# Optimization experiments

Measured on AMD Instinct MI355X. Metric: run time of the kernel, lower is better.

Reference implementation:

```python
import jax, jax.numpy as jnp
import numpy as np

D_MODEL = 1024
N_HEADS = 16
HEAD_DIM = D_MODEL // N_HEADS
SCALE = float(np.sqrt(HEAD_DIM))
NEG_INF = -1e30


def setup_inputs() -> dict:
    key = jax.random.key(0)
    k1, k2, k3 = jax.random.split(key, 3)
    B, S = 4, 2048
    x = jax.random.normal(k1, (B, S, D_MODEL), dtype=jnp.float32)
    attention_mask = jnp.ones((B, S), dtype=jnp.int32)
    # torch Linear(d, 3d, bias=False): y = x @ W^T; store pre-transposed (d, 3d)
    w_qkv = jax.random.normal(k2, (D_MODEL, 3 * D_MODEL), dtype=jnp.float32) * (1.0 / np.sqrt(D_MODEL))
    w_out = jax.random.normal(k3, (D_MODEL, D_MODEL), dtype=jnp.float32) * (1.0 / np.sqrt(D_MODEL))
    return {"x": x, "attention_mask": attention_mask, "w_qkv": w_qkv, "w_out": w_out}


def reference(x, attention_mask, w_qkv, w_out):
    B, S, _ = x.shape
    qkv = jnp.einsum('bsd,de->bse', x, w_qkv)                     # (B,S,3D)
    qkv = qkv.reshape(B, S, 3, N_HEADS, HEAD_DIM)
    q = qkv[:, :, 0].transpose(0, 2, 1, 3)                        # (B,H,S,hd)
    k = qkv[:, :, 1].transpose(0, 2, 1, 3)
    v = qkv[:, :, 2].transpose(0, 2, 1, 3)

    scores = jnp.einsum('bhqd,bhkd->bhqk', q, k) / SCALE          # (B,H,S,S)
    causal_mask = jnp.triu(jnp.ones((S, S), dtype=bool), k=1)     # True above diag
    scores = jnp.where(causal_mask[None, None], NEG_INF, scores)
    pad_mask = (attention_mask == 0)[:, None, None, :]            # (B,1,1,S)
    scores = jnp.where(pad_mask, NEG_INF, scores)

    attn = jax.nn.softmax(scores, axis=-1)                        # dropout=0 (eval)
    out = jnp.einsum('bhqk,bhkd->bhqd', attn, v)                  # (B,H,S,hd)
    out = out.transpose(0, 2, 1, 3).reshape(B, S, D_MODEL)
    return jnp.einsum('bsd,de->bse', out, w_out)
```

## Files before the change

### kernel.cpp

```cpp
#include <hip/hip_runtime.h>


typedef __attribute__((ext_vector_type(8))) short bf16x8;
typedef __attribute__((ext_vector_type(8))) unsigned short u16x8;
typedef __attribute__((ext_vector_type(4))) unsigned short u16x4;
typedef __attribute__((ext_vector_type(4))) float f32x4;

#define MFMA16 __builtin_amdgcn_mfma_f32_16x16x32_bf16

#define GLDS(gp, lp) __builtin_amdgcn_global_load_lds( \
    (const __attribute__((address_space(1))) unsigned int*)(gp), \
    (__attribute__((address_space(3))) unsigned int*)(lp), 16, 0, 0)

__device__ __forceinline__ unsigned short f2bf(float f) {
    union { float f; unsigned int u; } v; v.f = f;
    unsigned int r = v.u + 0x7fffu + ((v.u >> 16) & 1u);
    return (unsigned short)(r >> 16);
}

__global__ void k_prep(const float* __restrict__ x, unsigned short* __restrict__ xb,
                       const int* __restrict__ mask, unsigned short* __restrict__ mb,
                       const float* __restrict__ wqkv, unsigned short* __restrict__ w1t,
                       const float* __restrict__ wout, unsigned short* __restrict__ w2t) {
    __shared__ float tile[32][33];
    const int bx = blockIdx.x;
    if (bx < 4096) {
        size_t i = ((size_t)bx * 256 + threadIdx.x) * 8;
        float4 f0 = *(const float4*)(x + i);
        float4 f1 = *(const float4*)(x + i + 4);
        u16x8 v;
        v[0] = f2bf(f0.x); v[1] = f2bf(f0.y); v[2] = f2bf(f0.z); v[3] = f2bf(f0.w);
        v[4] = f2bf(f1.x); v[5] = f2bf(f1.y); v[6] = f2bf(f1.z); v[7] = f2bf(f1.w);
        *(u16x8*)(xb + i) = v;
        if (bx < 32) {
            int j = bx * 256 + threadIdx.x;
            mb[j] = mask[j] ? (unsigned short)0x3F80 : (unsigned short)0;
        }
    } else {
        const int b2 = bx - 4096;
        const int cb = b2 & 127, rb = b2 >> 7;
        const float* in = (cb < 96) ? wqkv : wout;
        unsigned short* out = (cb < 96) ? w1t : w2t;
        const int C = (cb < 96) ? 3072 : 1024;
        const int c0 = ((cb < 96) ? cb : cb - 96) * 32;
        const int r0 = rb * 32;
        int tx = threadIdx.x & 31, ty = threadIdx.x >> 5;
        for (int i = ty; i < 32; i += 8)
            tile[i][tx] = in[(size_t)(r0 + i) * C + (c0 + tx)];
        __syncthreads();
        for (int i = ty; i < 32; i += 8)
            out[(size_t)(c0 + i) * 1024 + (r0 + tx)] = f2bf(tile[tx][i]);
    }
}

template <int MODE>
__global__ __launch_bounds__(256) void k_gemm_bt(
    const unsigned short* __restrict__ Ab,
    const unsigned short* __restrict__ Bt,
    float* __restrict__ Cf,
    unsigned short* __restrict__ qb,
    unsigned short* __restrict__ kb,
    unsigned short* __restrict__ vt,
    const int* __restrict__ mask,
    int N, int K)
{
    __shared__ __align__(16) unsigned short la[128 * 64];
    __shared__ __align__(16) unsigned short lb[128 * 64];
    const int t = threadIdx.x;
    const int m0 = blockIdx.y * 128, n0 = blockIdx.x * 128;
    const int w = t >> 6, lane = t & 63;
    const int wm = (w & 1) * 64, wn = (w >> 1) * 64;
    const int lr = lane & 15, lq = lane >> 4;
    const int lr7 = lr & 7;
    const int rowb = lane >> 3;
    const int g8 = (((lane & 7) - rowb) & 7) * 8;

    f32x4 acc[4][4];
    for (int i = 0; i < 4; ++i)
        for (int j = 0; j < 4; ++j)
            acc[i][j] = (f32x4){0.f, 0.f, 0.f, 0.f};

    for (int k0 = 0; k0 < K; k0 += 64) {
        #pragma unroll
        for (int r = 0; r < 4; ++r) {
            const int rg = w * 8 + r * 32;
            GLDS(&Ab[(size_t)(m0 + rg + rowb) * K + k0 + g8], &la[rg * 64]);
            GLDS(&Bt[(size_t)(n0 + rg + rowb) * K + k0 + g8], &lb[rg * 64]);
        }
        __syncthreads();
        #pragma unroll
        for (int ks = 0; ks < 2; ++ks) {
            const int pa = ((ks * 4 + lq + lr7) & 7) * 8;
            bf16x8 af[4], bg[4];
            #pragma unroll
            for (int i = 0; i < 4; ++i) {
                af[i] = *(const bf16x8*)&la[(wm + i * 16 + lr) * 64 + pa];
                bg[i] = *(const bf16x8*)&lb[(wn + i * 16 + lr) * 64 + pa];
            }
            #pragma unroll
            for (int i = 0; i < 4; ++i)
                #pragma unroll
                for (int j = 0; j < 4; ++j)
                    acc[i][j] = MFMA16(af[i], bg[j], acc[i][j], 0, 0, 0);
        }
        __syncthreads();
    }

    const float QSCALE = 0.18033688f;
    if (MODE == 0) {
        for (int i = 0; i < 4; ++i)
            for (int j = 0; j < 4; ++j)
                for (int r = 0; r < 4; ++r) {
                    int row = m0 + wm + i * 16 + lq * 4 + r;
                    int col = n0 + wn + j * 16 + lr;
                    Cf[(size_t)row * N + col] = acc[i][j][r];
                }
    } else {
        const int which = n0 >> 10;
        if (which < 2) {
            unsigned short* dst = which ? kb : qb;
            const float sc = which ? 1.0f : QSCALE;
            for (int i = 0; i < 4; ++i)
                for (int j = 0; j < 4; ++j)
                    for (int r = 0; r < 4; ++r) {
                        int row = m0 + wm + i * 16 + lq * 4 + r;
                        int col = n0 + wn + j * 16 + lr;
                        int h = (col >> 6) & 15, d = col & 63;
                        int b = row >> 11, s = row & 2047;
                        dst[((size_t)(b * 16 + h) * 2048 + s) * 64 + d] = f2bf(acc[i][j][r] * sc);
                    }
        } else {
            for (int i = 0; i < 4; ++i) {
                int s0 = m0 + wm + i * 16 + lq * 4;
                int b = s0 >> 11, s = s0 & 2047;
                int4 m4 = *(const int4*)&mask[b * 2048 + s];
                for (int j = 0; j < 4; ++j) {
                    int col = n0 + wn + j * 16 + lr;
                    int h = (col >> 6) & 15, d = col & 63;
                    u16x4 pv;
                    pv[0] = m4.x ? f2bf(acc[i][j][0]) : (unsigned short)0;
                    pv[1] = m4.y ? f2bf(acc[i][j][1]) : (unsigned short)0;
                    pv[2] = m4.z ? f2bf(acc[i][j][2]) : (unsigned short)0;
                    pv[3] = m4.w ? f2bf(acc[i][j][3]) : (unsigned short)0;
                    *(u16x4*)&vt[((size_t)(b * 16 + h) * 64 + d) * 2048 + s] = pv;
                }
            }
        }
    }
}

__global__ __launch_bounds__(512, 4) void k_attn(
    const unsigned short* __restrict__ qb,
    const unsigned short* __restrict__ kb,
    const unsigned short* __restrict__ vt,
    const unsigned short* __restrict__ maskbg,
    unsigned short* __restrict__ ao)
{
    __shared__ __align__(16) unsigned short kt_lds[2][64 * 64];
    __shared__ __align__(16) unsigned short vt_lds[2][64 * 64];
    __shared__ __align__(16) unsigned short plds[8][16 * 72];

    const int t = threadIdx.x;
    const int w = t >> 6, lane = t & 63;
    const int lr = lane & 15, lq = lane >> 4;
    const int lr7 = lr & 7;
    const int bh = blockIdx.y, b = bh >> 4, h = bh & 15;

    const unsigned short* qp = qb + (size_t)bh * 2048 * 64;
    const unsigned short* kp = kb + (size_t)bh * 2048 * 64;
    const unsigned short* vp = vt + (size_t)bh * 64 * 2048;
    const unsigned short* mbg = maskbg + b * 2048;
    unsigned short* pw = plds[w];

    const int rowb = lane >> 3, c8 = lane & 7;
    const int sc8 = (c8 ^ rowb) * 8;

    auto stage = [&](int c) {
        const int buf = c & 1;
        const int k0 = c * 64;
        const int rg = 8 * w;
        const int row = rg + rowb;
        GLDS(&kp[(size_t)(k0 + row) * 64 + sc8], &kt_lds[buf][rg * 64]);
        GLDS(&vp[(size_t)row * 2048 + k0 + sc8], &vt_lds[buf][rg * 64]);
    };

    for (int pass = 0; pass < 2; ++pass) {
        const int stripe = pass ? (15 - (int)blockIdx.x) : (int)blockIdx.x;
        const int q0w = stripe * 128 + w * 16;

        bf16x8 aq0 = *(const bf16x8*)&qp[(q0w + lr) * 64 + lq * 8];
        bf16x8 aq1 = *(const bf16x8*)&qp[(q0w + lr) * 64 + 32 + lq * 8];

        f32x4 acc[4], lacc;
        lacc = (f32x4){0.f, 0.f, 0.f, 0.f};
        #pragma unroll
        for (int j = 0; j < 4; ++j) acc[j] = (f32x4){0.f, 0.f, 0.f, 0.f};

        const int nch = 2 * (stripe + 1);
        stage(0);
        for (int c = 0; c < nch; ++c) {
            __syncthreads();
            if (c + 1 < nch) stage(c + 1);
            const int k0 = c * 64;
            if (k0 < q0w + 16) {
                const unsigned short* kt = kt_lds[c & 1];
                const unsigned short* vtl = vt_lds[c & 1];
                const bool causal = (k0 + 63 > q0w);
                const int kcol0 = (lq ^ lr7) * 8;
                const int kcol1 = ((4 + lq) ^ lr7) * 8;
                #pragma unroll
                for (int ki = 0; ki < 4; ++ki) {
                    bf16x8 kf0 = *(const bf16x8*)&kt[(ki * 16 + lr) * 64 + kcol0];
                    bf16x8 kf1 = *(const bf16x8*)&kt[(ki * 16 + lr) * 64 + kcol1];
                    f32x4 s = (f32x4){0.f, 0.f, 0.f, 0.f};
                    s = MFMA16(kf0, aq0, s, 0, 0, 0);
                    s = MFMA16(kf1, aq1, s, 0, 0, 0);
                    unsigned int u[4];
                    #pragma unroll
                    for (int r = 0; r < 4; ++r) {
                        float scv = s[r];
                        if (causal) {
                            int key = k0 + ki * 16 + lq * 4 + r;
                            int qq  = q0w + lr;
                            scv = (key <= qq) ? scv : -3.0e38f;
                        }
                        float p = __builtin_amdgcn_exp2f(scv);
                        union { float f; unsigned int u; } cv; cv.f = p;
                        u[r] = cv.u;
                    }
                    uint2 pk;
                    pk.x = __builtin_amdgcn_perm(u[1], u[0], 0x07060302u);
                    pk.y = __builtin_amdgcn_perm(u[3], u[2], 0x07060302u);
                    *(uint2*)&pw[lr * 72 + ki * 16 + lq * 4] = pk;
                }
                #pragma unroll
                for (int kc = 0; kc < 64; kc += 32) {
                    bf16x8 pf = *(const bf16x8*)&pw[lr * 72 + kc + lq * 8];
                    bf16x8 mb = *(const bf16x8*)&mbg[k0 + kc + lq * 8];
                    const int vcol = (((kc >> 3) + lq) ^ lr7) * 8;
                    #pragma unroll
                    for (int j = 0; j < 4; ++j) {
                        bf16x8 vf = *(const bf16x8*)&vtl[(j * 16 + lr) * 64 + vcol];
                        acc[j] = MFMA16(pf, vf, acc[j], 0, 0, 0);
                    }
                    lacc = MFMA16(pf, mb, lacc, 0, 0, 0);
                }
            }
        }

        #pragma unroll
        for (int r = 0; r < 4; ++r) {
            float inv = 1.0f / fmaxf(lacc[r], 1e-30f);
            int row = q0w + lq * 4 + r;
            #pragma unroll
            for (int j = 0; j < 4; ++j) {
                int d = j * 16 + lr;
                ao[(size_t)(b * 2048 + row) * 1024 + h * 64 + d] = f2bf(acc[j][r] * inv);
            }
        }
        __syncthreads();
    }
}

extern "C" void kernel_launch(void* const* d_in, const int* in_sizes, int n_in,
                              void* d_out, int out_size, void* d_ws, size_t ws_size,
                              hipStream_t stream)
{
    const float* x    = (const float*)d_in[0];
    const int*   mask = (const int*)d_in[1];
    const float* wqkv = (const float*)d_in[2];
    const float* wout = (const float*)d_in[3];
    float* out = (float*)d_out;

    const size_t NEED = ((size_t)8192 * 1024 + (size_t)3072 * 1024 + (size_t)1024 * 1024 +
                         3 * (size_t)64 * 2048 * 64 + (size_t)8192 * 1024 + 8192) * 2;
    if (ws_size < NEED) return;

    char* ws = (char*)d_ws;
    unsigned short* xb  = (unsigned short*)ws; ws += (size_t)8192 * 1024 * 2;
    unsigned short* w1t = (unsigned short*)ws; ws += (size_t)3072 * 1024 * 2;
    unsigned short* w2t = (unsigned short*)ws; ws += (size_t)1024 * 1024 * 2;
    unsigned short* qb  = (unsigned short*)ws; ws += (size_t)64 * 2048 * 64 * 2;
    unsigned short* kb  = (unsigned short*)ws; ws += (size_t)64 * 2048 * 64 * 2;
    unsigned short* vt  = (unsigned short*)ws; ws += (size_t)64 * 64 * 2048 * 2;
    unsigned short* ao  = (unsigned short*)ws; ws += (size_t)8192 * 1024 * 2;
    unsigned short* mbg = (unsigned short*)ws; ws += (size_t)8192 * 2;

    k_prep<<<dim3(8192), 256, 0, stream>>>(x, xb, mask, mbg, wqkv, w1t, wout, w2t);
    k_gemm_bt<1><<<dim3(24, 64), 256, 0, stream>>>(xb, w1t, nullptr, qb, kb, vt, mask, 3072, 1024);
    k_attn<<<dim3(8, 64), 512, 0, stream>>>(qb, kb, vt, mbg, ao);
    k_gemm_bt<0><<<dim3(8, 64), 256, 0, stream>>>(ao, w2t, out, nullptr, nullptr, nullptr, nullptr, 1024, 1024);
}
```

Baseline: 254.4 us.

## Switch attention to 32x32x16 MFMA with 4 waves of 32 query rows

```diff
diff --git a/kernel.cpp b/kernel.cpp
--- a/kernel.cpp
+++ b/kernel.cpp
@@ -5,8 +5,10 @@
 typedef __attribute__((ext_vector_type(8))) unsigned short u16x8;
 typedef __attribute__((ext_vector_type(4))) unsigned short u16x4;
 typedef __attribute__((ext_vector_type(4))) float f32x4;
+typedef __attribute__((ext_vector_type(16))) float f32x16;
 
 #define MFMA16 __builtin_amdgcn_mfma_f32_16x16x32_bf16
+#define MFMA32 __builtin_amdgcn_mfma_f32_32x32x16_bf16
 
 #define GLDS(gp, lp) __builtin_amdgcn_global_load_lds( \
     (const __attribute__((address_space(1))) unsigned int*)(gp), \
@@ -149,7 +151,7 @@
     }
 }
 
-__global__ __launch_bounds__(512, 4) void k_attn(
+__global__ __launch_bounds__(256, 3) void k_attn(
     const unsigned short* __restrict__ qb,
     const unsigned short* __restrict__ kb,
     const unsigned short* __restrict__ vt,
@@ -158,12 +160,12 @@
 {
     __shared__ __align__(16) unsigned short kt_lds[2][64 * 64];
     __shared__ __align__(16) unsigned short vt_lds[2][64 * 64];
-    __shared__ __align__(16) unsigned short plds[8][16 * 72];
+    __shared__ __align__(16) unsigned short plds[4][32 * 72];
 
     const int t = threadIdx.x;
     const int w = t >> 6, lane = t & 63;
-    const int lr = lane & 15, lq = lane >> 4;
-    const int lr7 = lr & 7;
+    const int l31 = lane & 31, lh = lane >> 5;
+    const int l7 = l31 & 7;
     const int bh = blockIdx.y, b = bh >> 4, h = bh & 15;
 
     const unsigned short* qp = qb + (size_t)bh * 2048 * 64;
@@ -178,23 +180,28 @@
     auto stage = [&](int c) {
         const int buf = c & 1;
         const int k0 = c * 64;
-        const int rg = 8 * w;
-        const int row = rg + rowb;
-        GLDS(&kp[(size_t)(k0 + row) * 64 + sc8], &kt_lds[buf][rg * 64]);
-        GLDS(&vp[(size_t)row * 2048 + k0 + sc8], &vt_lds[buf][rg * 64]);
+        #pragma unroll
+        for (int r = 0; r < 2; ++r) {
+            const int rg = 8 * (w + 4 * r);
+            const int row = rg + rowb;
+            GLDS(&kp[(size_t)(k0 + row) * 64 + sc8], &kt_lds[buf][rg * 64]);
+            GLDS(&vp[(size_t)row * 2048 + k0 + sc8], &vt_lds[buf][rg * 64]);
+        }
     };
 
     for (int pass = 0; pass < 2; ++pass) {
         const int stripe = pass ? (15 - (int)blockIdx.x) : (int)blockIdx.x;
-        const int q0w = stripe * 128 + w * 16;
-
-        bf16x8 aq0 = *(const bf16x8*)&qp[(q0w + lr) * 64 + lq * 8];
-        bf16x8 aq1 = *(const bf16x8*)&qp[(q0w + lr) * 64 + 32 + lq * 8];
-
-        f32x4 acc[4], lacc;
-        lacc = (f32x4){0.f, 0.f, 0.f, 0.f};
-        #pragma unroll
-        for (int j = 0; j < 4; ++j) acc[j] = (f32x4){0.f, 0.f, 0.f, 0.f};
+        const int q0w = stripe * 128 + w * 32;
+
+        bf16x8 aq[4];
+        #pragma unroll
+        for (int ks = 0; ks < 4; ++ks)
+            aq[ks] = *(const bf16x8*)&qp[(q0w + l31) * 64 + ks * 16 + lh * 8];
+
+        f32x16 acc[2];
+        f32x16 lacc;
+        #pragma unroll
+        for (int r = 0; r < 16; ++r) { acc[0][r] = 0.f; acc[1][r] = 0.f; lacc[r] = 0.f; }
 
         const int nch = 2 * (stripe + 1);
         stage(0);
@@ -202,60 +209,68 @@
             __syncthreads();
             if (c + 1 < nch) stage(c + 1);
             const int k0 = c * 64;
-            if (k0 < q0w + 16) {
+            if (k0 < q0w + 32) {
                 const unsigned short* kt = kt_lds[c & 1];
                 const unsigned short* vtl = vt_lds[c & 1];
                 const bool causal = (k0 + 63 > q0w);
-                const int kcol0 = (lq ^ lr7) * 8;
-                const int kcol1 = ((4 + lq) ^ lr7) * 8;
+                bf16x8 mbf[4];
                 #pragma unroll
-                for (int ki = 0; ki < 4; ++ki) {
-                    bf16x8 kf0 = *(const bf16x8*)&kt[(ki * 16 + lr) * 64 + kcol0];
-                    bf16x8 kf1 = *(const bf16x8*)&kt[(ki * 16 + lr) * 64 + kcol1];
-                    f32x4 s = (f32x4){0.f, 0.f, 0.f, 0.f};
-                    s = MFMA16(kf0, aq0, s, 0, 0, 0);
-                    s = MFMA16(kf1, aq1, s, 0, 0, 0);
-                    unsigned int u[4];
-                    #pragma unroll
-                    for (int r = 0; r < 4; ++r) {
+                for (int ks = 0; ks < 4; ++ks)
+                    mbf[ks] = *(const bf16x8*)&mbg[k0 + ks * 16 + lh * 8];
+
+                #pragma unroll
+                for (int kt2 = 0; kt2 < 2; ++kt2) {
+                    f32x16 s;
+                    #pragma unroll
+                    for (int r = 0; r < 16; ++r) s[r] = 0.f;
+                    #pragma unroll
+                    for (int ks = 0; ks < 4; ++ks) {
+                        const int kb16 = ((ks * 2 + lh) ^ l7) * 8;
+                        bf16x8 kf = *(const bf16x8*)&kt[(kt2 * 32 + l31) * 64 + kb16];
+                        s = MFMA32(kf, aq[ks], s, 0, 0, 0);
+                    }
+                    unsigned int u[16];
+                    #pragma unroll
+                    for (int r = 0; r < 16; ++r) {
                         float scv = s[r];
                         if (causal) {
-                            int key = k0 + ki * 16 + lq * 4 + r;
-                            int qq  = q0w + lr;
-                            scv = (key <= qq) ? scv : -3.0e38f;
+                            int key = k0 + kt2 * 32 + (r & 3) + 8 * (r >> 2) + 4 * lh;
+                            scv = (key <= q0w + l31) ? scv : -3.0e38f;
                         }
                         float p = __builtin_amdgcn_exp2f(scv);
                         union { float f; unsigned int u; } cv; cv.f = p;
                         u[r] = cv.u;
                     }
-                    uint2 pk;
-                    pk.x = __builtin_amdgcn_perm(u[1], u[0], 0x07060302u);
-                    pk.y = __builtin_amdgcn_perm(u[3], u[2], 0x07060302u);
-                    *(uint2*)&pw[lr * 72 + ki * 16 + lq * 4] = pk;
+                    #pragma unroll
+                    for (int g = 0; g < 4; ++g) {
+                        uint2 pk;
+                        pk.x = __builtin_amdgcn_perm(u[4 * g + 1], u[4 * g], 0x07060302u);
+                        pk.y = __builtin_amdgcn_perm(u[4 * g + 3], u[4 * g + 2], 0x07060302u);
+                        *(uint2*)&pw[l31 * 72 + kt2 * 32 + g * 8 + 4 * lh] = pk;
+                    }
                 }
                 #pragma unroll
-                for (int kc = 0; kc < 64; kc += 32) {
-                    bf16x8 pf = *(const bf16x8*)&pw[lr * 72 + kc + lq * 8];
-                    bf16x8 mb = *(const bf16x8*)&mbg[k0 + kc + lq * 8];
-                    const int vcol = (((kc >> 3) + lq) ^ lr7) * 8;
-                    #pragma unroll
-                    for (int j = 0; j < 4; ++j) {
-                        bf16x8 vf = *(const bf16x8*)&vtl[(j * 16 + lr) * 64 + vcol];
-                        acc[j] = MFMA16(pf, vf, acc[j], 0, 0, 0);
-                    }
-                    lacc = MFMA16(pf, mb, lacc, 0, 0, 0);
+                for (int ks = 0; ks < 4; ++ks) {
+                    bf16x8 pf = *(const bf16x8*)&pw[l31 * 72 + ks * 16 + lh * 8];
+                    const int vb16 = ((ks * 2 + lh) ^ l7) * 8;
+                    #pragma unroll
+                    for (int j = 0; j < 2; ++j) {
+                        bf16x8 vf = *(const bf16x8*)&vtl[(j * 32 + l31) * 64 + vb16];
+                        acc[j] = MFMA32(pf, vf, acc[j], 0, 0, 0);
+                    }
+                    lacc = MFMA32(pf, mbf[ks], lacc, 0, 0, 0);
                 }
             }
         }
 
         #pragma unroll
-        for (int r = 0; r < 4; ++r) {
+        for (int r = 0; r < 16; ++r) {
             float inv = 1.0f / fmaxf(lacc[r], 1e-30f);
-            int row = q0w + lq * 4 + r;
+            int qq = q0w + (r & 3) + 8 * (r >> 2) + 4 * lh;
             #pragma unroll
-            for (int j = 0; j < 4; ++j) {
-                int d = j * 16 + lr;
-                ao[(size_t)(b * 2048 + row) * 1024 + h * 64 + d] = f2bf(acc[j][r] * inv);
+            for (int j = 0; j < 2; ++j) {
+                int d = j * 32 + l31;
+                ao[(size_t)(b * 2048 + qq) * 1024 + h * 64 + d] = f2bf(acc[j][r] * inv);
             }
         }
         __syncthreads();
@@ -288,6 +303,6 @@
 
     k_prep<<<dim3(8192), 256, 0, stream>>>(x, xb, mask, mbg, wqkv, w1t, wout, w2t);
     k_gemm_bt<1><<<dim3(24, 64), 256, 0, stream>>>(xb, w1t, nullptr, qb, kb, vt, mask, 3072, 1024);
-    k_attn<<<dim3(8, 64), 512, 0, stream>>>(qb, kb, vt, mbg, ao);
+    k_attn<<<dim3(8, 64), 256, 0, stream>>>(qb, kb, vt, mbg, ao);
     k_gemm_bt<0><<<dim3(8, 64), 256, 0, stream>>>(ao, w2t, out, nullptr, nullptr, nullptr, nullptr, 1024, 1024);
 }
```

Result: slower. 260.1 us (+2.3%).

## Shrink attention tiles to 64-query stripes and 32-key chunks with 4-wave blocks

Applied to the files above, without the earlier changes.

```diff
diff --git a/kernel.cpp b/kernel.cpp
--- a/kernel.cpp
+++ b/kernel.cpp
@@ -149,22 +149,22 @@
     }
 }
 
-__global__ __launch_bounds__(512, 4) void k_attn(
+__global__ __launch_bounds__(256, 4) void k_attn(
     const unsigned short* __restrict__ qb,
     const unsigned short* __restrict__ kb,
     const unsigned short* __restrict__ vt,
     const unsigned short* __restrict__ maskbg,
     unsigned short* __restrict__ ao)
 {
-    __shared__ __align__(16) unsigned short kt_lds[2][64 * 64];
-    __shared__ __align__(16) unsigned short vt_lds[2][64 * 64];
-    __shared__ __align__(16) unsigned short plds[8][16 * 72];
+    __shared__ __align__(16) unsigned short kt_lds[2][32 * 64];
+    __shared__ __align__(16) unsigned short vt_lds[2][64 * 32];
+    __shared__ __align__(16) unsigned short plds[4][16 * 40];
 
     const int t = threadIdx.x;
     const int w = t >> 6, lane = t & 63;
     const int lr = lane & 15, lq = lane >> 4;
     const int lr7 = lr & 7;
-    const int bh = blockIdx.y, b = bh >> 4, h = bh & 15;
+    const int bh = blockIdx.x, b = bh >> 4, h = bh & 15;
 
     const unsigned short* qp = qb + (size_t)bh * 2048 * 64;
     const unsigned short* kp = kb + (size_t)bh * 2048 * 64;
@@ -172,21 +172,23 @@
     const unsigned short* mbg = maskbg + b * 2048;
     unsigned short* pw = plds[w];
 
-    const int rowb = lane >> 3, c8 = lane & 7;
-    const int sc8 = (c8 ^ rowb) * 8;
+    const int krow = lane >> 3, kblk = lane & 7;
+    const int kcol = (kblk ^ krow) * 8;
+    const int vrow = lane >> 2, vcol = (lane & 3) * 8;
 
     auto stage = [&](int c) {
         const int buf = c & 1;
-        const int k0 = c * 64;
-        const int rg = 8 * w;
-        const int row = rg + rowb;
-        GLDS(&kp[(size_t)(k0 + row) * 64 + sc8], &kt_lds[buf][rg * 64]);
-        GLDS(&vp[(size_t)row * 2048 + k0 + sc8], &vt_lds[buf][rg * 64]);
+        const int k0 = c * 32;
+        GLDS(&kp[(size_t)(k0 + 8 * w + krow) * 64 + kcol], &kt_lds[buf][(8 * w) * 64]);
+        GLDS(&vp[(size_t)(16 * w + vrow) * 2048 + k0 + vcol], &vt_lds[buf][(16 * w) * 32]);
     };
 
+    const int pa0 = (lq ^ lr7) * 8;
+    const int pa1 = ((4 + lq) ^ lr7) * 8;
+
     for (int pass = 0; pass < 2; ++pass) {
-        const int stripe = pass ? (15 - (int)blockIdx.x) : (int)blockIdx.x;
-        const int q0w = stripe * 128 + w * 16;
+        const int stripe = pass ? (31 - (int)blockIdx.y) : (int)blockIdx.y;
+        const int q0w = stripe * 64 + w * 16;
 
         bf16x8 aq0 = *(const bf16x8*)&qp[(q0w + lr) * 64 + lq * 8];
         bf16x8 aq1 = *(const bf16x8*)&qp[(q0w + lr) * 64 + 32 + lq * 8];
@@ -201,17 +203,15 @@
         for (int c = 0; c < nch; ++c) {
             __syncthreads();
             if (c + 1 < nch) stage(c + 1);
-            const int k0 = c * 64;
+            const int k0 = c * 32;
             if (k0 < q0w + 16) {
                 const unsigned short* kt = kt_lds[c & 1];
                 const unsigned short* vtl = vt_lds[c & 1];
-                const bool causal = (k0 + 63 > q0w);
-                const int kcol0 = (lq ^ lr7) * 8;
-                const int kcol1 = ((4 + lq) ^ lr7) * 8;
+                const bool causal = (k0 + 31 > q0w);
                 #pragma unroll
-                for (int ki = 0; ki < 4; ++ki) {
-                    bf16x8 kf0 = *(const bf16x8*)&kt[(ki * 16 + lr) * 64 + kcol0];
-                    bf16x8 kf1 = *(const bf16x8*)&kt[(ki * 16 + lr) * 64 + kcol1];
+                for (int ki = 0; ki < 2; ++ki) {
+                    bf16x8 kf0 = *(const bf16x8*)&kt[(ki * 16 + lr) * 64 + pa0];
+                    bf16x8 kf1 = *(const bf16x8*)&kt[(ki * 16 + lr) * 64 + pa1];
                     f32x4 s = (f32x4){0.f, 0.f, 0.f, 0.f};
                     s = MFMA16(kf0, aq0, s, 0, 0, 0);
                     s = MFMA16(kf1, aq1, s, 0, 0, 0);
@@ -221,8 +221,7 @@
                         float scv = s[r];
                         if (causal) {
                             int key = k0 + ki * 16 + lq * 4 + r;
-                            int qq  = q0w + lr;
-                            scv = (key <= qq) ? scv : -3.0e38f;
+                            scv = (key <= q0w + lr) ? scv : -3.0e38f;
                         }
                         float p = __builtin_amdgcn_exp2f(scv);
                         union { float f; unsigned int u; } cv; cv.f = p;
@@ -231,20 +230,16 @@
                     uint2 pk;
                     pk.x = __builtin_amdgcn_perm(u[1], u[0], 0x07060302u);
                     pk.y = __builtin_amdgcn_perm(u[3], u[2], 0x07060302u);
-                    *(uint2*)&pw[lr * 72 + ki * 16 + lq * 4] = pk;
-                }
+                    *(uint2*)&pw[lr * 40 + ki * 16 + lq * 4] = pk;
+                }
+                bf16x8 pf = *(const bf16x8*)&pw[lr * 40 + lq * 8];
+                bf16x8 mb = *(const bf16x8*)&mbg[k0 + lq * 8];
                 #pragma unroll
-                for (int kc = 0; kc < 64; kc += 32) {
-                    bf16x8 pf = *(const bf16x8*)&pw[lr * 72 + kc + lq * 8];
-                    bf16x8 mb = *(const bf16x8*)&mbg[k0 + kc + lq * 8];
-                    const int vcol = (((kc >> 3) + lq) ^ lr7) * 8;
-                    #pragma unroll
-                    for (int j = 0; j < 4; ++j) {
-                        bf16x8 vf = *(const bf16x8*)&vtl[(j * 16 + lr) * 64 + vcol];
-                        acc[j] = MFMA16(pf, vf, acc[j], 0, 0, 0);
-                    }
-                    lacc = MFMA16(pf, mb, lacc, 0, 0, 0);
-                }
+                for (int j = 0; j < 4; ++j) {
+                    bf16x8 vf = *(const bf16x8*)&vtl[(j * 16 + lr) * 32 + lq * 8];
+                    acc[j] = MFMA16(pf, vf, acc[j], 0, 0, 0);
+                }
+                lacc = MFMA16(pf, mb, lacc, 0, 0, 0);
             }
         }
 
@@ -288,6 +283,6 @@
 
     k_prep<<<dim3(8192), 256, 0, stream>>>(x, xb, mask, mbg, wqkv, w1t, wout, w2t);
     k_gemm_bt<1><<<dim3(24, 64), 256, 0, stream>>>(xb, w1t, nullptr, qb, kb, vt, mask, 3072, 1024);
-    k_attn<<<dim3(8, 64), 512, 0, stream>>>(qb, kb, vt, mbg, ao);
+    k_attn<<<dim3(64, 16), 256, 0, stream>>>(qb, kb, vt, mbg, ao);
     k_gemm_bt<0><<<dim3(8, 64), 256, 0, stream>>>(ao, w2t, out, nullptr, nullptr, nullptr, nullptr, 1024, 1024);
 }
```

New measurement: 252.7 us. Within noise of the previous version (-0.6%).
